# Optimization experiments

Measured on AMD Instinct MI355X. Metric: run time of the kernel, lower is better.

The kernel has to match this reference:

```python
import jax, jax.numpy as jnp
import numpy as np

V, H, B, T = 32000, 1024, 32, 256  # vocab, rnn_size, batch, seq_length


def setup_inputs() -> dict:
    key = jax.random.key(0)
    ks = jax.random.split(key, 6)
    s = 1.0 / np.sqrt(H)
    return {
        "input_data": jax.random.randint(ks[0], (B, T), 0, V, dtype=jnp.int32),
        "targets": jax.random.randint(ks[1], (B, T), 0, V, dtype=jnp.int32),
        "embedding": jax.random.uniform(ks[2], (V, H), minval=-1.0, maxval=1.0, dtype=jnp.float32),
        "softmax_b": jnp.zeros((V,), jnp.float32),
        "W0": (jax.random.normal(ks[3], (2 * H, 4 * H)) * s).astype(jnp.float32),
        "b0": jnp.zeros((4 * H,), jnp.float32),
        "W1": (jax.random.normal(ks[4], (2 * H, 4 * H)) * s).astype(jnp.float32),
        "b1": jnp.zeros((4 * H,), jnp.float32),
    }


def _lstm_step(x, c, h, W, b):
    # TF LSTMCell: gates i, j, f, o; forget_bias = 1.0
    z = jnp.concatenate([x, h], axis=-1) @ W + b  # [B, 4H]
    i, j, f, o = jnp.split(z, 4, axis=-1)
    c2 = c * jax.nn.sigmoid(f + 1.0) + jax.nn.sigmoid(i) * jnp.tanh(j)
    h2 = jax.nn.sigmoid(o) * jnp.tanh(c2)
    return c2, h2


def reference(input_data, targets, embedding, softmax_b, W0, b0, W1, b1):
    x = embedding[input_data]  # [B, T, H]
    Bb, Hh = x.shape[0], embedding.shape[1]
    zeros = jnp.zeros((Bb, Hh), x.dtype)
    init = ((zeros, zeros), (zeros, zeros))  # ((c0,h0),(c1,h1))

    def step(carry, xt):
        (c0, h0), (c1, h1) = carry
        c0, h0 = _lstm_step(xt, c0, h0, W0, b0)
        c1, h1 = _lstm_step(h0, c1, h1, W1, b1)
        return ((c0, h0), (c1, h1)), h1

    _, outs = jax.lax.scan(step, init, jnp.swapaxes(x, 0, 1))  # [T, B, H]
    output = jnp.swapaxes(outs, 0, 1).reshape(-1, Hh)  # [B*T, H]
    logits = output @ embedding.T + softmax_b  # tied softmax weights, [B*T, V]
    labels = targets.reshape(-1)
    logp = jax.nn.log_softmax(logits)
    loss = -jnp.take_along_axis(logp, labels[:, None], axis=1)[:, 0]
    cost = jnp.sum(loss) / Bb
    return logits, cost
```

## Files before the change

kernel.cpp:

```cpp
#include <hip/hip_runtime.h>
#include <hip/hip_bf16.h>

#define DEV static __device__ __forceinline__

typedef unsigned short u16;
typedef unsigned long long u64;
typedef __attribute__((ext_vector_type(8))) short short8;
typedef __attribute__((ext_vector_type(4))) float f32x4;

constexpr int V = 32000, H = 1024, B = 32, T = 256;
constexpr int BT = B * T;
constexpr int G  = 4 * H;
constexpr int NCH = V / 256;
constexpr int NWG2 = 256;
constexpr int RSTRIDE = 32 * 2048 + 2048;

constexpr size_t SZ_WT    = (size_t)G * 2048 * 2;
constexpr size_t OFF_W0T  = 0;
constexpr size_t OFF_W1T  = OFF_W0T + SZ_WT;
constexpr size_t OFF_EBF  = OFF_W1T + SZ_WT;
constexpr size_t OFF_XBF  = OFF_EBF + (size_t)V * H * 2;
constexpr size_t OFF_XP0  = OFF_XBF + (size_t)BT * H * 2;
constexpr size_t OFF_H1   = OFF_XP0 + (size_t)BT * G * 2;
constexpr size_t OFF_HSEQ = OFF_H1 + (size_t)BT * H * 2;
constexpr size_t SZ_HSEQ  = (size_t)(T + 2) * RSTRIDE * 2;
constexpr size_t OFF_SYNC = OFF_HSEQ + SZ_HSEQ;
constexpr size_t SZ_SYNC  = (size_t)2 * 256 * 128 * 4;
constexpr size_t OFF_PMAX = OFF_SYNC + SZ_SYNC;
constexpr size_t OFF_PSUM = OFF_PMAX + (size_t)BT * NCH * 4;
constexpr size_t OFF_LOSS = OFF_PSUM + (size_t)BT * NCH * 4;

DEV u16 f2bf(float x) {
  union { float f; unsigned int u; } v; v.f = x;
  unsigned int r = v.u + 0x7fffu + ((v.u >> 16) & 1u);
  return (u16)(r >> 16);
}
DEV float bf2f(u16 b) {
  union { unsigned int u; float f; } v; v.u = ((unsigned int)b) << 16;
  return v.f;
}
DEV float sigm(float x) { return 1.f / (1.f + expf(-x)); }

DEV void gload_lds16(const u16* g, u16* l) {
  __builtin_amdgcn_global_load_lds(
      (__attribute__((address_space(1))) void*)g,
      (__attribute__((address_space(3))) void*)l, 16, 0, 0);
}


__global__ void k_transpose_cvt(const float* __restrict__ in, u16* __restrict__ out,
                                int R, int C) {
  __shared__ float tile[32][33];
  int bc = blockIdx.x * 32, br = blockIdx.y * 32;
  int tx = threadIdx.x & 31, ty0 = threadIdx.x >> 5;
#pragma unroll
  for (int i = 0; i < 4; ++i) {
    int ty = ty0 + i * 8;
    tile[ty][tx] = in[(size_t)(br + ty) * C + bc + tx];
  }
  __syncthreads();
#pragma unroll
  for (int i = 0; i < 4; ++i) {
    int ty = ty0 + i * 8;
    out[(size_t)(bc + ty) * R + br + tx] = f2bf(tile[tx][ty]);
  }
}

__global__ void k_cvt_bf16(const float* __restrict__ in, u16* __restrict__ out, int n4) {
  int i = blockIdx.x * blockDim.x + threadIdx.x;
  int stride = gridDim.x * blockDim.x;
  for (; i < n4; i += stride) {
    float4 v = ((const float4*)in)[i];
    ushort4 o;
    o.x = f2bf(v.x); o.y = f2bf(v.y); o.z = f2bf(v.z); o.w = f2bf(v.w);
    ((ushort4*)out)[i] = o;
  }
}

__global__ void k_gather_x(const float* __restrict__ emb, const int* __restrict__ inp,
                           u16* __restrict__ Xbf) {
  int row = blockIdx.x;
  int t = row >> 5, b = row & 31;
  int tok = inp[b * T + t];
  const float4* src = (const float4*)(emb + (size_t)tok * H);
  ushort4* dst = (ushort4*)(Xbf + (size_t)row * H);
  float4 v = src[threadIdx.x];
  ushort4 o;
  o.x = f2bf(v.x); o.y = f2bf(v.y); o.z = f2bf(v.z); o.w = f2bf(v.w);
  dst[threadIdx.x] = o;
}

__global__ void k_zero(unsigned int* __restrict__ p, int nwords) {
  int i = blockIdx.x * blockDim.x + threadIdx.x;
  int stride = gridDim.x * blockDim.x;
  for (; i < nwords; i += stride) p[i] = 0u;
}

template <int CMODE>
__global__ __launch_bounds__(256)
void k_gemm(const u16* __restrict__ A, int lda,
            const u16* __restrict__ Bt, int ldb,
            float* __restrict__ C, int ldc,
            const float* __restrict__ bias, int K) {
  __shared__ alignas(16) u16 ldsA[128 * 32];
  __shared__ alignas(16) u16 ldsB[128 * 32];

  unsigned nwg = gridDim.x * gridDim.y;
  unsigned flat = blockIdx.y * gridDim.x + blockIdx.x;
  unsigned nf = (flat & 7) * (nwg >> 3) + (flat >> 3);
  unsigned bx = nf % gridDim.x, by = nf / gridDim.x;

  int tid = threadIdx.x, lane = tid & 63, w = tid >> 6;
  int row0 = by * 128, col0 = bx * 128;
  int wr = w >> 1, wc = w & 1;
  int c15 = lane & 15, q4 = lane >> 4;

  const u16* ag[2]; const u16* bg[2];
#pragma unroll
  for (int j = 0; j < 2; ++j) {
    int r = (j * 4 + w) * 16 + (lane >> 2);
    int k = (lane & 3) * 8;
    ag[j] = A + (size_t)(row0 + r) * lda + k;
    bg[j] = Bt + (size_t)(col0 + r) * ldb + k;
  }
  u16* lA0 = ldsA + (size_t)(0 + w) * 512;
  u16* lA1 = ldsA + (size_t)(4 + w) * 512;
  u16* lB0 = ldsB + (size_t)(0 + w) * 512;
  u16* lB1 = ldsB + (size_t)(4 + w) * 512;

  f32x4 acc[4][4];
#pragma unroll
  for (int m = 0; m < 4; ++m)
#pragma unroll
    for (int n = 0; n < 4; ++n) acc[m][n] = (f32x4){0.f, 0.f, 0.f, 0.f};

  int nk = K >> 5;
  for (int kk = 0; kk < nk; ++kk) {
    int kb = kk * 32;
    gload_lds16(ag[0] + kb, lA0);
    gload_lds16(ag[1] + kb, lA1);
    gload_lds16(bg[0] + kb, lB0);
    gload_lds16(bg[1] + kb, lB1);
    __syncthreads();

    short8 af[4], bfr[4];
#pragma unroll
    for (int m = 0; m < 4; ++m)
      af[m] = *(const short8*)(ldsA + (wr * 64 + m * 16 + c15) * 32 + q4 * 8);
#pragma unroll
    for (int n = 0; n < 4; ++n)
      bfr[n] = *(const short8*)(ldsB + (wc * 64 + n * 16 + c15) * 32 + q4 * 8);
#pragma unroll
    for (int m = 0; m < 4; ++m)
#pragma unroll
      for (int n = 0; n < 4; ++n)
        acc[m][n] = __builtin_amdgcn_mfma_f32_16x16x32_bf16(af[m], bfr[n], acc[m][n], 0, 0, 0);
    __syncthreads();
  }

  float bias_n[4];
#pragma unroll
  for (int n = 0; n < 4; ++n) bias_n[n] = bias[col0 + wc * 64 + n * 16 + c15];

#pragma unroll
  for (int m = 0; m < 4; ++m) {
#pragma unroll
    for (int jr = 0; jr < 4; ++jr) {
      int r_g = row0 + wr * 64 + m * 16 + q4 * 4 + jr;
#pragma unroll
      for (int n = 0; n < 4; ++n) {
        int c_g = col0 + wc * 64 + n * 16 + c15;
        float val = acc[m][n][jr] + bias_n[n];
        if (CMODE == 0) {
          C[(size_t)r_g * ldc + c_g] = val;
        } else {
          int tt = r_g >> 5, bb = r_g & 31;
          int q = c_g >> 10, wgup = (c_g & 1023) >> 3, uu = c_g & 7;
          ((u16*)C)[((((size_t)tt * 128 + wgup) * 32 + bb) * 32) + q * 8 + uu] = f2bf(val);
        }
      }
    }
  }
}

constexpr int GNT = 32;

DEV void stage_half256(const u16* __restrict__ A, int lda,
                       const u16* __restrict__ Bt, int ldb,
                       int row0, int col0, u16* lds, int Hh, int tid) {
  int t = Hh >> 2, j = Hh & 3, op = j >> 1, hh = j & 1;
  int wid = tid >> 6, lane = tid & 63;
  int r = hh * 128 + wid * 16 + (lane >> 2);
  int k = t * 32 + (((lane & 3) ^ ((lane >> 2) & 3)) << 3);
  const u16* g = (op == 0) ? (A + (size_t)(row0 + r) * lda + k)
                           : (Bt + (size_t)(col0 + r) * ldb + k);
  u16* l = lds + (size_t)((op * 2 + (t & 1)) * 8192 + (hh * 128 + wid * 16) * 32);
  gload_lds16(g, l);
}

template <bool SM_EPI>
__global__ __launch_bounds__(512)
void k_gemm256(const u16* __restrict__ A, int lda,
               const u16* __restrict__ Bt, int ldb,
               float* __restrict__ C, int ldc,
               const float* __restrict__ bias,
               float* __restrict__ pmax, float* __restrict__ psum, int nch) {
  __shared__ alignas(16) u16 lds[4 * 8192];

  unsigned nwg = gridDim.x * gridDim.y;
  unsigned flat = blockIdx.y * gridDim.x + blockIdx.x;
  unsigned nf = (flat & 7) * (nwg >> 3) + (flat >> 3);
  int bx = nf % gridDim.x, by = nf / gridDim.x;
  int row0 = by * 256, col0 = bx * 256;

  int tid = threadIdx.x, lane = tid & 63, wid = tid >> 6;
  int wr = wid >> 2, wc = wid & 3;
  int c15 = lane & 15, q4 = lane >> 4;
  int usw = (q4 ^ (c15 & 3)) << 3;

  f32x4 acc[8][4];
#pragma unroll
  for (int m = 0; m < 8; ++m)
#pragma unroll
    for (int n = 0; n < 4; ++n) acc[m][n] = (f32x4){0.f, 0.f, 0.f, 0.f};

#pragma unroll
  for (int h = 0; h < 7; ++h)
    stage_half256(A, lda, Bt, ldb, row0, col0, lds, h, tid);
  asm volatile("s_waitcnt vmcnt(3)" ::: "memory");
  __builtin_amdgcn_sched_barrier(0);
  __builtin_amdgcn_s_barrier();

  int Hh = 7;
  short8 af[4], bfr[4];

  for (int t = 0; t < GNT; ++t) {
    int pt = t & 1;
    const u16* la = lds + pt * 8192;
    const u16* lb = lds + (2 + pt) * 8192;

#pragma unroll
    for (int m = 0; m < 4; ++m)
      af[m] = *(const short8*)(la + (wr * 128 + m * 16 + c15) * 32 + usw);
#pragma unroll
    for (int n = 0; n < 4; ++n)
      bfr[n] = *(const short8*)(lb + (wc * 64 + n * 16 + c15) * 32 + usw);
    if (Hh < 4 * GNT) { stage_half256(A, lda, Bt, ldb, row0, col0, lds, Hh, tid); ++Hh; }
    if (Hh < 4 * GNT) { stage_half256(A, lda, Bt, ldb, row0, col0, lds, Hh, tid); ++Hh; }
    __builtin_amdgcn_s_barrier();
    asm volatile("s_waitcnt lgkmcnt(0)" ::: "memory");
    __builtin_amdgcn_sched_barrier(0);
    __builtin_amdgcn_s_setprio(1);
#pragma unroll
    for (int m = 0; m < 4; ++m)
#pragma unroll
      for (int n = 0; n < 4; ++n)
        acc[m][n] = __builtin_amdgcn_mfma_f32_16x16x32_bf16(af[m], bfr[n], acc[m][n], 0, 0, 0);
    __builtin_amdgcn_s_setprio(0);
    __builtin_amdgcn_s_barrier();

#pragma unroll
    for (int m = 0; m < 4; ++m)
      af[m] = *(const short8*)(la + (wr * 128 + (m + 4) * 16 + c15) * 32 + usw);
    if (Hh < 4 * GNT) { stage_half256(A, lda, Bt, ldb, row0, col0, lds, Hh, tid); ++Hh; }
    if (Hh < 4 * GNT) { stage_half256(A, lda, Bt, ldb, row0, col0, lds, Hh, tid); ++Hh; }
    __builtin_amdgcn_s_barrier();
    asm volatile("s_waitcnt lgkmcnt(0)" ::: "memory");
    __builtin_amdgcn_sched_barrier(0);
    __builtin_amdgcn_s_setprio(1);
#pragma unroll
    for (int m = 0; m < 4; ++m)
#pragma unroll
      for (int n = 0; n < 4; ++n)
        acc[m + 4][n] = __builtin_amdgcn_mfma_f32_16x16x32_bf16(af[m], bfr[n], acc[m + 4][n], 0, 0, 0);
    __builtin_amdgcn_s_setprio(0);
    if (t < GNT - 2) {
      asm volatile("s_waitcnt vmcnt(3)" ::: "memory");
      __builtin_amdgcn_sched_barrier(0);
    } else if (t == GNT - 2) {
      asm volatile("s_waitcnt vmcnt(0)" ::: "memory");
      __builtin_amdgcn_sched_barrier(0);
    }
    __builtin_amdgcn_s_barrier();
  }

  float bias_n[4];
#pragma unroll
  for (int n = 0; n < 4; ++n) bias_n[n] = bias[col0 + wc * 64 + n * 16 + c15];

  float2* red = (float2*)lds;
  __syncthreads();

#pragma unroll
  for (int m = 0; m < 8; ++m) {
#pragma unroll
    for (int jr = 0; jr < 4; ++jr) {
      int rloc = wr * 128 + m * 16 + q4 * 4 + jr;
      int r_g = row0 + rloc;
      float v[4];
#pragma unroll
      for (int n = 0; n < 4; ++n) {
        int c_g = col0 + wc * 64 + n * 16 + c15;
        float val = acc[m][n][jr] + bias_n[n];
        C[(size_t)r_g * ldc + c_g] = val;
        v[n] = val;
      }
      if (SM_EPI) {
        float mx = fmaxf(fmaxf(v[0], v[1]), fmaxf(v[2], v[3]));
        float s = __expf(v[0] - mx) + __expf(v[1] - mx) + __expf(v[2] - mx) + __expf(v[3] - mx);
#pragma unroll
        for (int d = 1; d < 16; d <<= 1) {
          float mo = __shfl_xor(mx, d, 64);
          float so = __shfl_xor(s, d, 64);
          float M2 = fmaxf(mx, mo);
          s = s * __expf(mx - M2) + so * __expf(mo - M2);
          mx = M2;
        }
        if (c15 == 0) red[rloc * 4 + wc] = make_float2(mx, s);
      }
    }
  }
  if (SM_EPI) {
    __syncthreads();
    if (tid < 256) {
      float M = -1e30f, S = 0.f;
#pragma unroll
      for (int i = 0; i < 4; ++i) {
        float2 a = red[tid * 4 + i];
        float M2 = fmaxf(M, a.x);
        S = S * __expf(M - M2) + a.y * __expf(a.x - M2);
        M = M2;
      }
      pmax[(size_t)(row0 + tid) * nch + bx] = M;
      psum[(size_t)(row0 + tid) * nch + bx] = S;
    }
  }
}


#define RED(w_, bt_, nt_, r_, c_) red[((((w_)*2 + (bt_)) * 2 + (nt_)) * 16 + (r_)) * 16 + (c_)]

DEV void wait_flags(const int* __restrict__ fa, const int* __restrict__ fb) {
  if (threadIdx.x < 64) {
    int lane = threadIdx.x;
    while (true) {
      int ok = 1;
      if (fa) {
        int a0 = __hip_atomic_load(fa + lane,      __ATOMIC_RELAXED, __HIP_MEMORY_SCOPE_AGENT);
        int a1 = __hip_atomic_load(fa + 64 + lane, __ATOMIC_RELAXED, __HIP_MEMORY_SCOPE_AGENT);
        ok &= (a0 != 0) & (a1 != 0);
      }
      if (fb) {
        int b0 = __hip_atomic_load(fb + lane,      __ATOMIC_RELAXED, __HIP_MEMORY_SCOPE_AGENT);
        int b1 = __hip_atomic_load(fb + 64 + lane, __ATOMIC_RELAXED, __HIP_MEMORY_SCOPE_AGENT);
        ok &= (b0 != 0) & (b1 != 0);
      }
      if (__all(ok)) break;
      __builtin_amdgcn_s_sleep(1);
    }
  }
  __builtin_amdgcn_sched_barrier(0);
  __syncthreads();
}

DEV void publish_flag(int* __restrict__ word) {
  __syncthreads();
  if (threadIdx.x == 0)
    __hip_atomic_store(word, 1, __ATOMIC_RELAXED, __HIP_MEMORY_SCOPE_AGENT);
}

template <int KH, bool IS_L0>
DEV void lstm_role(const u16* __restrict__ WT,
                   const u16* __restrict__ xp0p,
                   const float* __restrict__ zb1,
                   u16* __restrict__ hseq, u16* __restrict__ H1bf,
                   int* __restrict__ f0, int* __restrict__ f1,
                   float* __restrict__ red, int wgu) {
  constexpr int KOFF = IS_L0 ? 1024 : 0;
  constexpr int KS = KH / 4;
  constexpr int NKC = KS / 32;
  int tid = threadIdx.x, lane = tid & 63, w = tid >> 6;
  int c15 = lane & 15, q4 = lane >> 4;
  int eb = tid >> 3, eu = tid & 7;

  short8 wfr[2][NKC];
#pragma unroll
  for (int nt = 0; nt < 2; ++nt) {
    int lr = nt * 16 + c15;
    const u16* rp = WT + (size_t)((lr >> 3) * 1024 + wgu * 8 + (lr & 7)) * 2048
                    + KOFF + w * KS + q4 * 8;
#pragma unroll
    for (int kc = 0; kc < NKC; ++kc)
      wfr[nt][kc] = *(const short8*)(rp + kc * 32);
  }

  float zpc[4];
  if (!IS_L0) {
#pragma unroll
    for (int q = 0; q < 4; ++q) zpc[q] = zb1[q * 1024 + wgu * 8 + eu];
  }
  float creg = 0.f;

  for (int it_t = 0; it_t < T; ++it_t) {
    int t = IS_L0 ? it_t : it_t + 1;

    float zp[4];
    if (IS_L0) {
#pragma unroll
      for (int q = 0; q < 4; ++q)
        zp[q] = bf2f(xp0p[((((size_t)t * 128 + wgu) * 32 + eb) * 32) + q * 8 + eu]);
    } else {
#pragma unroll
      for (int q = 0; q < 4; ++q) zp[q] = zpc[q];
    }

    if (IS_L0) {
      if (t >= 1) wait_flags(f0 + (size_t)(t - 1) * 128, nullptr);
    } else {
      wait_flags(f0 + (size_t)(t - 1) * 128,
                 t >= 2 ? f1 + (size_t)(t - 2) * 128 : nullptr);
    }

    const u16* hread = hseq + (size_t)t * RSTRIDE;
    f32x4 acc[2][2];
#pragma unroll
    for (int bt = 0; bt < 2; ++bt)
#pragma unroll
      for (int nt = 0; nt < 2; ++nt) acc[bt][nt] = (f32x4){0.f, 0.f, 0.f, 0.f};

#pragma unroll
    for (int kc = 0; kc < NKC; ++kc) {
      int kh = w * KS + kc * 32 + q4 * 8;
      short8 a0 = *(const short8*)(hread + (size_t)c15 * 2048 + kh);
      short8 a1 = *(const short8*)(hread + (size_t)(16 + c15) * 2048 + kh);
      acc[0][0] = __builtin_amdgcn_mfma_f32_16x16x32_bf16(a0, wfr[0][kc], acc[0][0], 0, 0, 0);
      acc[0][1] = __builtin_amdgcn_mfma_f32_16x16x32_bf16(a0, wfr[1][kc], acc[0][1], 0, 0, 0);
      acc[1][0] = __builtin_amdgcn_mfma_f32_16x16x32_bf16(a1, wfr[0][kc], acc[1][0], 0, 0, 0);
      acc[1][1] = __builtin_amdgcn_mfma_f32_16x16x32_bf16(a1, wfr[1][kc], acc[1][1], 0, 0, 0);
    }

#pragma unroll
    for (int bt = 0; bt < 2; ++bt)
#pragma unroll
      for (int nt = 0; nt < 2; ++nt)
#pragma unroll
        for (int jr = 0; jr < 4; ++jr)
          RED(w, bt, nt, q4 * 4 + jr, c15) = acc[bt][nt][jr];
    __syncthreads();

    int bt = eb >> 4, rr = eb & 15;
    float z[4];
#pragma unroll
    for (int q = 0; q < 4; ++q) {
      int lr = q * 8 + eu, nt = lr >> 4, cc = lr & 15;
      z[q] = RED(0, bt, nt, rr, cc) + RED(1, bt, nt, rr, cc) +
             RED(2, bt, nt, rr, cc) + RED(3, bt, nt, rr, cc) + zp[q];
    }
    float gi = sigm(z[0]);
    float gj = tanhf(z[1]);
    float gf = sigm(z[2] + 1.f);
    float go = sigm(z[3]);
    creg = creg * gf + gi * gj;
    float hv = go * tanhf(creg);

    int hb = (int)f2bf(hv);
    int hp = __shfl_xor(hb, 1, 64);
    if (!(tid & 1)) {
      unsigned int pack = (unsigned int)(u16)hb | ((unsigned int)(u16)hp << 16);
      u16* hwr = hseq + (size_t)(t + 1) * RSTRIDE + (IS_L0 ? 0 : 1024);
      __hip_atomic_store((unsigned int*)(hwr + (size_t)eb * 2048 + wgu * 8 + eu), pack,
                         __ATOMIC_RELAXED, __HIP_MEMORY_SCOPE_AGENT);
      if (!IS_L0)
        __builtin_nontemporal_store(pack,
            (unsigned int*)(H1bf + ((size_t)eb * T + (t - 1)) * H + wgu * 8 + eu));
    }

    publish_flag(IS_L0 ? (f0 + (size_t)t * 128 + wgu)
                       : (f1 + (size_t)(t - 1) * 128 + wgu));
  }
}

__global__ __launch_bounds__(256, 1)
void k_lstm_persistent(const u16* __restrict__ W0T, const u16* __restrict__ W1T,
                       const u16* __restrict__ xp0p, const float* __restrict__ b1,
                       u16* __restrict__ hseq, u16* __restrict__ H1bf,
                       int* __restrict__ sync) {
  __shared__ float red[4 * 2 * 2 * 16 * 16];
  int* f0 = sync;
  int* f1 = sync + 256 * 128;
  int wg = blockIdx.x;
  if (wg < 128)
    lstm_role<1024, true>(W0T, xp0p, nullptr, hseq, H1bf, f0, f1, red, wg);
  else
    lstm_role<2048, false>(W1T, nullptr, b1, hseq, H1bf, f0, f1, red, wg - 128);
}

__global__ void k_rowfin(const float* __restrict__ pmax, const float* __restrict__ psum,
                         const float* __restrict__ Cl, const int* __restrict__ targets,
                         float* __restrict__ loss) {
  int row = blockIdx.x;
  int tid = threadIdx.x, lane = tid & 63, w = tid >> 6;
  float mx = -1e30f, s = 0.f;
  if (tid < NCH) { mx = pmax[(size_t)row * NCH + tid]; s = psum[(size_t)row * NCH + tid]; }
#pragma unroll
  for (int d = 1; d < 64; d <<= 1) {
    float mo = __shfl_xor(mx, d, 64);
    float so = __shfl_xor(s, d, 64);
    float M2 = fmaxf(mx, mo);
    s = s * __expf(mx - M2) + so * __expf(mo - M2);
    mx = M2;
  }
  __shared__ float2 wred[4];
  if (lane == 0) wred[w] = make_float2(mx, s);
  __syncthreads();
  if (tid == 0) {
    float M = wred[0].x, S = wred[0].y;
#pragma unroll
    for (int i = 1; i < 4; ++i) {
      float M2 = fmaxf(M, wred[i].x);
      S = S * __expf(M - M2) + wred[i].y * __expf(wred[i].x - M2);
      M = M2;
    }
    float logZ = M + logf(S);
    int tgt = targets[row];
    float xt = Cl[(size_t)row * V + tgt];
    loss[row] = logZ - xt;
  }
}

__global__ void k_cost(const float* __restrict__ loss, float* __restrict__ out) {
  int tid = threadIdx.x, lane = tid & 63, w = tid >> 6;
  float s = 0.f;
  for (int i = tid; i < BT; i += 256) s += loss[i];
#pragma unroll
  for (int d = 1; d < 64; d <<= 1) s += __shfl_xor(s, d, 64);
  __shared__ float ws4[4];
  if (lane == 0) ws4[w] = s;
  __syncthreads();
  if (tid == 0) out[0] = (ws4[0] + ws4[1] + ws4[2] + ws4[3]) * (1.0f / B);
}

extern "C" void kernel_launch(void* const* d_in, const int* in_sizes, int n_in,
                              void* d_out, int out_size, void* d_ws, size_t ws_size,
                              hipStream_t stream) {
  const int*   input_data = (const int*)d_in[0];
  const int*   targets    = (const int*)d_in[1];
  const float* emb        = (const float*)d_in[2];
  const float* softmax_b  = (const float*)d_in[3];
  const float* W0         = (const float*)d_in[4];
  const float* b0         = (const float*)d_in[5];
  const float* W1         = (const float*)d_in[6];
  const float* b1         = (const float*)d_in[7];
  float* out = (float*)d_out;
  char*  ws  = (char*)d_ws;

  u16*   W0T  = (u16*)(ws + OFF_W0T);
  u16*   W1T  = (u16*)(ws + OFF_W1T);
  u16*   Ebf  = (u16*)(ws + OFF_EBF);
  u16*   Xbf  = (u16*)(ws + OFF_XBF);
  u16*   xp0p = (u16*)(ws + OFF_XP0);
  u16*   H1bf = (u16*)(ws + OFF_H1);
  u16*   hseq = (u16*)(ws + OFF_HSEQ);
  int*   sync = (int*)(ws + OFF_SYNC);
  float* pmax = (float*)(ws + OFF_PMAX);
  float* psum = (float*)(ws + OFF_PSUM);
  float* lossb= (float*)(ws + OFF_LOSS);

  k_transpose_cvt<<<dim3(G / 32, 2048 / 32), 256, 0, stream>>>(W0, W0T, 2048, G);
  k_transpose_cvt<<<dim3(G / 32, 2048 / 32), 256, 0, stream>>>(W1, W1T, 2048, G);
  k_cvt_bf16<<<2048, 256, 0, stream>>>(emb, Ebf, V * H / 4);
  k_gather_x<<<BT, 256, 0, stream>>>(emb, input_data, Xbf);
  k_zero<<<64, 256, 0, stream>>>((unsigned int*)(ws + OFF_HSEQ), RSTRIDE);
  k_zero<<<64, 256, 0, stream>>>((unsigned int*)(ws + OFF_SYNC), (int)(SZ_SYNC / 4));

  k_gemm<1><<<dim3(G / 128, BT / 128), 256, 0, stream>>>(
      Xbf, H, W0T, 2048, (float*)xp0p, G, b0, H);

  k_lstm_persistent<<<dim3(NWG2), dim3(256), 0, stream>>>(
      W0T, W1T, xp0p, b1, hseq, H1bf, sync);

  k_gemm256<true><<<dim3(V / 256, BT / 256), 512, 0, stream>>>(
      H1bf, H, Ebf, H, out, V, softmax_b, pmax, psum, NCH);

  k_rowfin<<<BT, 256, 0, stream>>>(pmax, psum, out, targets, lossb);
  k_cost<<<1, 256, 0, stream>>>(lossb, out + (size_t)BT * V);
}
```

Measured before the change: 2.991 ms.

## Split LSTM batch into two independent chains and triple-buffer logits GEMM LDS

The persistent LSTM kernel now processes the batch as two independent 16-row halves, each with its own hidden-state buffer and flag arrays. One half's matmul and gate work can proceed while the other half waits on its inter-workgroup flags, hiding part of the per-step synchronization latency. The cost is twice as many flag waits and barriers per timestep, with the gate epilogue running on only half the threads. Separately, the vocab-projection GEMM moves from double to triple LDS buffering with a two-tile prefetch distance, at the cost of more shared memory per block.

```diff
diff --git a/kernel.cpp b/kernel.cpp
--- a/kernel.cpp
+++ b/kernel.cpp
@@ -13,7 +13,7 @@
 constexpr int G  = 4 * H;
 constexpr int NCH = V / 256;
 constexpr int NWG2 = 256;
-constexpr int RSTRIDE = 32 * 2048 + 2048;
+constexpr int RST2 = 16 * 2048 + 1024;
 
 constexpr size_t SZ_WT    = (size_t)G * 2048 * 2;
 constexpr size_t OFF_W0T  = 0;
@@ -23,9 +23,9 @@
 constexpr size_t OFF_XP0  = OFF_XBF + (size_t)BT * H * 2;
 constexpr size_t OFF_H1   = OFF_XP0 + (size_t)BT * G * 2;
 constexpr size_t OFF_HSEQ = OFF_H1 + (size_t)BT * H * 2;
-constexpr size_t SZ_HSEQ  = (size_t)(T + 2) * RSTRIDE * 2;
+constexpr size_t SZ_HSEQ  = (size_t)2 * (T + 2) * RST2 * 2;
 constexpr size_t OFF_SYNC = OFF_HSEQ + SZ_HSEQ;
-constexpr size_t SZ_SYNC  = (size_t)2 * 256 * 128 * 4;
+constexpr size_t SZ_SYNC  = (size_t)2 * 2 * 256 * 128 * 4;
 constexpr size_t OFF_PMAX = OFF_SYNC + SZ_SYNC;
 constexpr size_t OFF_PSUM = OFF_PMAX + (size_t)BT * NCH * 4;
 constexpr size_t OFF_LOSS = OFF_PSUM + (size_t)BT * NCH * 4;
@@ -185,16 +185,16 @@
 
 constexpr int GNT = 32;
 
-DEV void stage_half256(const u16* __restrict__ A, int lda,
-                       const u16* __restrict__ Bt, int ldb,
-                       int row0, int col0, u16* lds, int Hh, int tid) {
-  int t = Hh >> 2, j = Hh & 3, op = j >> 1, hh = j & 1;
+DEV void stage256(const u16* __restrict__ A, int lda,
+                  const u16* __restrict__ Bt, int ldb,
+                  int row0, int col0, u16* lds, int t, int h, int tid) {
+  int op = h >> 1, hh = h & 1;
   int wid = tid >> 6, lane = tid & 63;
   int r = hh * 128 + wid * 16 + (lane >> 2);
   int k = t * 32 + (((lane & 3) ^ ((lane >> 2) & 3)) << 3);
   const u16* g = (op == 0) ? (A + (size_t)(row0 + r) * lda + k)
                            : (Bt + (size_t)(col0 + r) * ldb + k);
-  u16* l = lds + (size_t)((op * 2 + (t & 1)) * 8192 + (hh * 128 + wid * 16) * 32);
+  u16* l = lds + (size_t)((op * 3 + (t % 3)) * 8192 + (hh * 128 + wid * 16) * 32);
   gload_lds16(g, l);
 }
 
@@ -205,7 +205,7 @@
                float* __restrict__ C, int ldc,
                const float* __restrict__ bias,
                float* __restrict__ pmax, float* __restrict__ psum, int nch) {
-  __shared__ alignas(16) u16 lds[4 * 8192];
+  __shared__ alignas(16) u16 lds[6 * 8192];
 
   unsigned nwg = gridDim.x * gridDim.y;
   unsigned flat = blockIdx.y * gridDim.x + blockIdx.x;
@@ -225,19 +225,18 @@
     for (int n = 0; n < 4; ++n) acc[m][n] = (f32x4){0.f, 0.f, 0.f, 0.f};
 
 #pragma unroll
-  for (int h = 0; h < 7; ++h)
-    stage_half256(A, lda, Bt, ldb, row0, col0, lds, h, tid);
-  asm volatile("s_waitcnt vmcnt(3)" ::: "memory");
+  for (int h = 0; h < 4; ++h) stage256(A, lda, Bt, ldb, row0, col0, lds, 0, h, tid);
+#pragma unroll
+  for (int h = 0; h < 4; ++h) stage256(A, lda, Bt, ldb, row0, col0, lds, 1, h, tid);
+  asm volatile("s_waitcnt vmcnt(4)" ::: "memory");
   __builtin_amdgcn_sched_barrier(0);
   __builtin_amdgcn_s_barrier();
 
-  int Hh = 7;
   short8 af[4], bfr[4];
 
   for (int t = 0; t < GNT; ++t) {
-    int pt = t & 1;
-    const u16* la = lds + pt * 8192;
-    const u16* lb = lds + (2 + pt) * 8192;
+    const u16* la = lds + (size_t)(t % 3) * 8192;
+    const u16* lb = lds + (size_t)(3 + t % 3) * 8192;
 
 #pragma unroll
     for (int m = 0; m < 4; ++m)
@@ -245,8 +244,10 @@
 #pragma unroll
     for (int n = 0; n < 4; ++n)
       bfr[n] = *(const short8*)(lb + (wc * 64 + n * 16 + c15) * 32 + usw);
-    if (Hh < 4 * GNT) { stage_half256(A, lda, Bt, ldb, row0, col0, lds, Hh, tid); ++Hh; }
-    if (Hh < 4 * GNT) { stage_half256(A, lda, Bt, ldb, row0, col0, lds, Hh, tid); ++Hh; }
+    if (t + 2 < GNT) {
+      stage256(A, lda, Bt, ldb, row0, col0, lds, t + 2, 0, tid);
+      stage256(A, lda, Bt, ldb, row0, col0, lds, t + 2, 1, tid);
+    }
     __builtin_amdgcn_s_barrier();
     asm volatile("s_waitcnt lgkmcnt(0)" ::: "memory");
     __builtin_amdgcn_sched_barrier(0);
@@ -262,8 +263,10 @@
 #pragma unroll
     for (int m = 0; m < 4; ++m)
       af[m] = *(const short8*)(la + (wr * 128 + (m + 4) * 16 + c15) * 32 + usw);
-    if (Hh < 4 * GNT) { stage_half256(A, lda, Bt, ldb, row0, col0, lds, Hh, tid); ++Hh; }
-    if (Hh < 4 * GNT) { stage_half256(A, lda, Bt, ldb, row0, col0, lds, Hh, tid); ++Hh; }
+    if (t + 2 < GNT) {
+      stage256(A, lda, Bt, ldb, row0, col0, lds, t + 2, 2, tid);
+      stage256(A, lda, Bt, ldb, row0, col0, lds, t + 2, 3, tid);
+    }
     __builtin_amdgcn_s_barrier();
     asm volatile("s_waitcnt lgkmcnt(0)" ::: "memory");
     __builtin_amdgcn_sched_barrier(0);
@@ -275,7 +278,7 @@
         acc[m + 4][n] = __builtin_amdgcn_mfma_f32_16x16x32_bf16(af[m], bfr[n], acc[m + 4][n], 0, 0, 0);
     __builtin_amdgcn_s_setprio(0);
     if (t < GNT - 2) {
-      asm volatile("s_waitcnt vmcnt(3)" ::: "memory");
+      asm volatile("s_waitcnt vmcnt(4)" ::: "memory");
       __builtin_amdgcn_sched_barrier(0);
     } else if (t == GNT - 2) {
       asm volatile("s_waitcnt vmcnt(0)" ::: "memory");
@@ -338,7 +341,7 @@
 }
 
 
-#define RED(w_, bt_, nt_, r_, c_) red[((((w_)*2 + (bt_)) * 2 + (nt_)) * 16 + (r_)) * 16 + (c_)]
+#define RED3(w_, nt_, r_, c_) red[(((w_)*2 + (nt_)) * 16 + (r_)) * 16 + (c_)]
 
 DEV void wait_flags(const int* __restrict__ fa, const int* __restrict__ fb) {
   if (threadIdx.x < 64) {
@@ -361,12 +364,6 @@
   }
   __builtin_amdgcn_sched_barrier(0);
   __syncthreads();
-}
-
-DEV void publish_flag(int* __restrict__ word) {
-  __syncthreads();
-  if (threadIdx.x == 0)
-    __hip_atomic_store(word, 1, __ATOMIC_RELAXED, __HIP_MEMORY_SCOPE_AGENT);
 }
 
 template <int KH, bool IS_L0>
@@ -381,7 +378,8 @@
   constexpr int NKC = KS / 32;
   int tid = threadIdx.x, lane = tid & 63, w = tid >> 6;
   int c15 = lane & 15, q4 = lane >> 4;
-  int eb = tid >> 3, eu = tid & 7;
+  int eb = (tid >> 3) & 15, eu = tid & 7;
+  bool epi = tid < 128;
 
   short8 wfr[2][NKC];
 #pragma unroll
@@ -399,95 +397,99 @@
 #pragma unroll
     for (int q = 0; q < 4; ++q) zpc[q] = zb1[q * 1024 + wgu * 8 + eu];
   }
-  float creg = 0.f;
+  float cregs[2] = {0.f, 0.f};
 
   for (int it_t = 0; it_t < T; ++it_t) {
     int t = IS_L0 ? it_t : it_t + 1;
-
-    float zp[4];
-    if (IS_L0) {
-#pragma unroll
-      for (int q = 0; q < 4; ++q)
-        zp[q] = bf2f(xp0p[((((size_t)t * 128 + wgu) * 32 + eb) * 32) + q * 8 + eu]);
-    } else {
-#pragma unroll
-      for (int q = 0; q < 4; ++q) zp[q] = zpc[q];
-    }
-
-    if (IS_L0) {
-      if (t >= 1) wait_flags(f0 + (size_t)(t - 1) * 128, nullptr);
-    } else {
-      wait_flags(f0 + (size_t)(t - 1) * 128,
-                 t >= 2 ? f1 + (size_t)(t - 2) * 128 : nullptr);
-    }
-
-    const u16* hread = hseq + (size_t)t * RSTRIDE;
-    f32x4 acc[2][2];
-#pragma unroll
-    for (int bt = 0; bt < 2; ++bt)
-#pragma unroll
-      for (int nt = 0; nt < 2; ++nt) acc[bt][nt] = (f32x4){0.f, 0.f, 0.f, 0.f};
-
-#pragma unroll
-    for (int kc = 0; kc < NKC; ++kc) {
-      int kh = w * KS + kc * 32 + q4 * 8;
-      short8 a0 = *(const short8*)(hread + (size_t)c15 * 2048 + kh);
-      short8 a1 = *(const short8*)(hread + (size_t)(16 + c15) * 2048 + kh);
-      acc[0][0] = __builtin_amdgcn_mfma_f32_16x16x32_bf16(a0, wfr[0][kc], acc[0][0], 0, 0, 0);
-      acc[0][1] = __builtin_amdgcn_mfma_f32_16x16x32_bf16(a0, wfr[1][kc], acc[0][1], 0, 0, 0);
-      acc[1][0] = __builtin_amdgcn_mfma_f32_16x16x32_bf16(a1, wfr[0][kc], acc[1][0], 0, 0, 0);
-      acc[1][1] = __builtin_amdgcn_mfma_f32_16x16x32_bf16(a1, wfr[1][kc], acc[1][1], 0, 0, 0);
-    }
-
-#pragma unroll
-    for (int bt = 0; bt < 2; ++bt)
-#pragma unroll
-      for (int nt = 0; nt < 2; ++nt)
-#pragma unroll
-        for (int jr = 0; jr < 4; ++jr)
-          RED(w, bt, nt, q4 * 4 + jr, c15) = acc[bt][nt][jr];
-    __syncthreads();
-
-    int bt = eb >> 4, rr = eb & 15;
-    float z[4];
-#pragma unroll
-    for (int q = 0; q < 4; ++q) {
-      int lr = q * 8 + eu, nt = lr >> 4, cc = lr & 15;
-      z[q] = RED(0, bt, nt, rr, cc) + RED(1, bt, nt, rr, cc) +
-             RED(2, bt, nt, rr, cc) + RED(3, bt, nt, rr, cc) + zp[q];
-    }
-    float gi = sigm(z[0]);
-    float gj = tanhf(z[1]);
-    float gf = sigm(z[2] + 1.f);
-    float go = sigm(z[3]);
-    creg = creg * gf + gi * gj;
-    float hv = go * tanhf(creg);
-
-    int hb = (int)f2bf(hv);
-    int hp = __shfl_xor(hb, 1, 64);
-    if (!(tid & 1)) {
-      unsigned int pack = (unsigned int)(u16)hb | ((unsigned int)(u16)hp << 16);
-      u16* hwr = hseq + (size_t)(t + 1) * RSTRIDE + (IS_L0 ? 0 : 1024);
-      __hip_atomic_store((unsigned int*)(hwr + (size_t)eb * 2048 + wgu * 8 + eu), pack,
-                         __ATOMIC_RELAXED, __HIP_MEMORY_SCOPE_AGENT);
-      if (!IS_L0)
-        __builtin_nontemporal_store(pack,
-            (unsigned int*)(H1bf + ((size_t)eb * T + (t - 1)) * H + wgu * 8 + eu));
-    }
-
-    publish_flag(IS_L0 ? (f0 + (size_t)t * 128 + wgu)
-                       : (f1 + (size_t)(t - 1) * 128 + wgu));
+#pragma unroll
+    for (int c = 0; c < 2; ++c) {
+      float zp[4];
+      if (IS_L0) {
+        int b = c * 16 + eb;
+#pragma unroll
+        for (int q = 0; q < 4; ++q)
+          zp[q] = bf2f(xp0p[((((size_t)t * 128 + wgu) * 32 + b) * 32) + q * 8 + eu]);
+      } else {
+#pragma unroll
+        for (int q = 0; q < 4; ++q) zp[q] = zpc[q];
+      }
+
+      if (IS_L0) {
+        if (t >= 1) wait_flags(f0 + ((size_t)c * 256 + (t - 1)) * 128, nullptr);
+      } else {
+        wait_flags(f0 + ((size_t)c * 256 + (t - 1)) * 128,
+                   t >= 2 ? f1 + ((size_t)c * 256 + (t - 2)) * 128 : nullptr);
+      }
+
+      const u16* hread = hseq + ((size_t)c * (T + 2) + t) * RST2;
+      short8 afr[NKC];
+#pragma unroll
+      for (int kc = 0; kc < NKC; ++kc)
+        afr[kc] = *(const short8*)(hread + (size_t)c15 * 2048 + w * KS + kc * 32 + q4 * 8);
+
+      f32x4 acc0 = (f32x4){0.f, 0.f, 0.f, 0.f};
+      f32x4 acc1 = (f32x4){0.f, 0.f, 0.f, 0.f};
+#pragma unroll
+      for (int kc = 0; kc < NKC; ++kc) {
+        acc0 = __builtin_amdgcn_mfma_f32_16x16x32_bf16(afr[kc], wfr[0][kc], acc0, 0, 0, 0);
+        acc1 = __builtin_amdgcn_mfma_f32_16x16x32_bf16(afr[kc], wfr[1][kc], acc1, 0, 0, 0);
+      }
+
+#pragma unroll
+      for (int jr = 0; jr < 4; ++jr) {
+        RED3(w, 0, q4 * 4 + jr, c15) = acc0[jr];
+        RED3(w, 1, q4 * 4 + jr, c15) = acc1[jr];
+      }
+      __syncthreads();
+
+      if (epi) {
+        float z[4];
+#pragma unroll
+        for (int q = 0; q < 4; ++q) {
+          int lr = q * 8 + eu, nt = lr >> 4, cc = lr & 15;
+          z[q] = RED3(0, nt, eb, cc) + RED3(1, nt, eb, cc) +
+                 RED3(2, nt, eb, cc) + RED3(3, nt, eb, cc) + zp[q];
+        }
+        float gi = sigm(z[0]);
+        float gj = tanhf(z[1]);
+        float gf = sigm(z[2] + 1.f);
+        float go = sigm(z[3]);
+        cregs[c] = cregs[c] * gf + gi * gj;
+        float hv = go * tanhf(cregs[c]);
+
+        int hb = (int)f2bf(hv);
+        int hp = __shfl_xor(hb, 1, 64);
+        if (!(tid & 1)) {
+          unsigned int pack = (unsigned int)(u16)hb | ((unsigned int)(u16)hp << 16);
+          u16* hwr = hseq + ((size_t)c * (T + 2) + t + 1) * RST2 + (IS_L0 ? 0 : 1024);
+          __hip_atomic_store((unsigned int*)(hwr + (size_t)eb * 2048 + wgu * 8 + eu), pack,
+                             __ATOMIC_RELAXED, __HIP_MEMORY_SCOPE_AGENT);
+          if (!IS_L0) {
+            int b = c * 16 + eb;
+            __builtin_nontemporal_store(pack,
+                (unsigned int*)(H1bf + ((size_t)b * T + (t - 1)) * H + wgu * 8 + eu));
+          }
+        }
+      }
+
+      __syncthreads();
+      if (tid == 0) {
+        int* word = IS_L0 ? (f0 + ((size_t)c * 256 + t) * 128 + wgu)
+                          : (f1 + ((size_t)c * 256 + (t - 1)) * 128 + wgu);
+        __hip_atomic_store(word, 1, __ATOMIC_RELAXED, __HIP_MEMORY_SCOPE_AGENT);
+      }
+    }
   }
 }
 
 __global__ __launch_bounds__(256, 1)
-void k_lstm_persistent(const u16* __restrict__ W0T, const u16* __restrict__ W1T,
-                       const u16* __restrict__ xp0p, const float* __restrict__ b1,
-                       u16* __restrict__ hseq, u16* __restrict__ H1bf,
-                       int* __restrict__ sync) {
-  __shared__ float red[4 * 2 * 2 * 16 * 16];
+void k_lstm3(const u16* __restrict__ W0T, const u16* __restrict__ W1T,
+             const u16* __restrict__ xp0p, const float* __restrict__ b1,
+             u16* __restrict__ hseq, u16* __restrict__ H1bf,
+             int* __restrict__ sync) {
+  __shared__ float red[4 * 2 * 16 * 16];
   int* f0 = sync;
-  int* f1 = sync + 256 * 128;
+  int* f1 = sync + 2 * 256 * 128;
   int wg = blockIdx.x;
   if (wg < 128)
     lstm_role<1024, true>(W0T, xp0p, nullptr, hseq, H1bf, f0, f1, red, wg);
@@ -570,13 +572,15 @@
   k_transpose_cvt<<<dim3(G / 32, 2048 / 32), 256, 0, stream>>>(W1, W1T, 2048, G);
   k_cvt_bf16<<<2048, 256, 0, stream>>>(emb, Ebf, V * H / 4);
   k_gather_x<<<BT, 256, 0, stream>>>(emb, input_data, Xbf);
-  k_zero<<<64, 256, 0, stream>>>((unsigned int*)(ws + OFF_HSEQ), RSTRIDE);
+  k_zero<<<32, 256, 0, stream>>>((unsigned int*)(ws + OFF_HSEQ), RST2);
+  k_zero<<<32, 256, 0, stream>>>(
+      (unsigned int*)(ws + OFF_HSEQ + (size_t)(T + 2) * RST2 * 2), RST2);
   k_zero<<<64, 256, 0, stream>>>((unsigned int*)(ws + OFF_SYNC), (int)(SZ_SYNC / 4));
 
   k_gemm<1><<<dim3(G / 128, BT / 128), 256, 0, stream>>>(
       Xbf, H, W0T, 2048, (float*)xp0p, G, b0, H);
 
-  k_lstm_persistent<<<dim3(NWG2), dim3(256), 0, stream>>>(
+  k_lstm3<<<dim3(NWG2), dim3(256), 0, stream>>>(
       W0T, W1T, xp0p, b1, hseq, H1bf, sync);
 
   k_gemm256<true><<<dim3(V / 256, BT / 256), 512, 0, stream>>>(
```

Result: no change. 2.993 ms (+0.1%).

## Triple-buffer GEMM pipeline, reuse it for input projection, merge and slim small kernels

Applied to the files above, without the earlier changes.

The 256-tile GEMM moves from a double-buffered LDS ring with a half-tile stage counter to a triple-buffered ring that prefetches two K-steps ahead. The same kernel now also handles the layer-0 input projection, replacing the smaller 128-tile GEMM. The two weight-transpose launches become one launch using blockIdx.z. The LSTM spin-wait drops its s_sleep, and k_rowfin now gives each row one wavefront with no LDS reduction. Together these aim to cut pipeline stalls, launch count and idle polling, at the cost of more LDS per block (which may lower occupancy) and busier spinning.

```diff
diff --git a/kernel.cpp b/kernel.cpp
--- a/kernel.cpp
+++ b/kernel.cpp
@@ -48,21 +48,23 @@
 }
 
 
-__global__ void k_transpose_cvt(const float* __restrict__ in, u16* __restrict__ out,
-                                int R, int C) {
+__global__ void k_transpose_cvt2(const float* __restrict__ in0, u16* __restrict__ out0,
+                                 const float* __restrict__ in1, u16* __restrict__ out1) {
+  const float* in = blockIdx.z ? in1 : in0;
+  u16* out = blockIdx.z ? out1 : out0;
   __shared__ float tile[32][33];
   int bc = blockIdx.x * 32, br = blockIdx.y * 32;
   int tx = threadIdx.x & 31, ty0 = threadIdx.x >> 5;
 #pragma unroll
   for (int i = 0; i < 4; ++i) {
     int ty = ty0 + i * 8;
-    tile[ty][tx] = in[(size_t)(br + ty) * C + bc + tx];
+    tile[ty][tx] = in[(size_t)(br + ty) * G + bc + tx];
   }
   __syncthreads();
 #pragma unroll
   for (int i = 0; i < 4; ++i) {
     int ty = ty0 + i * 8;
-    out[(size_t)(bc + ty) * R + br + tx] = f2bf(tile[tx][ty]);
+    out[(size_t)(bc + ty) * 2048 + br + tx] = f2bf(tile[tx][ty]);
   }
 }
 
@@ -96,216 +98,138 @@
   for (; i < nwords; i += stride) p[i] = 0u;
 }
 
-template <int CMODE>
-__global__ __launch_bounds__(256)
-void k_gemm(const u16* __restrict__ A, int lda,
-            const u16* __restrict__ Bt, int ldb,
-            float* __restrict__ C, int ldc,
-            const float* __restrict__ bias, int K) {
-  __shared__ alignas(16) u16 ldsA[128 * 32];
-  __shared__ alignas(16) u16 ldsB[128 * 32];
+constexpr int GNT = 32;
+
+DEV void stage256(const u16* __restrict__ A, int lda,
+                  const u16* __restrict__ Bt, int ldb,
+                  int row0, int col0, u16* lds, int t, int h, int tid) {
+  int op = h >> 1, hh = h & 1;
+  int wid = tid >> 6, lane = tid & 63;
+  int r = hh * 128 + wid * 16 + (lane >> 2);
+  int k = t * 32 + (((lane & 3) ^ ((lane >> 2) & 3)) << 3);
+  const u16* g = (op == 0) ? (A + (size_t)(row0 + r) * lda + k)
+                           : (Bt + (size_t)(col0 + r) * ldb + k);
+  u16* l = lds + (size_t)((op * 3 + (t % 3)) * 8192 + (hh * 128 + wid * 16) * 32);
+  gload_lds16(g, l);
+}
+
+template <int MODE>
+__global__ __launch_bounds__(512)
+void k_gemm256(const u16* __restrict__ A, int lda,
+               const u16* __restrict__ Bt, int ldb,
+               float* __restrict__ C, int ldc,
+               const float* __restrict__ bias,
+               float* __restrict__ pmax, float* __restrict__ psum, int nch) {
+  __shared__ alignas(16) u16 lds[6 * 8192];
 
   unsigned nwg = gridDim.x * gridDim.y;
   unsigned flat = blockIdx.y * gridDim.x + blockIdx.x;
   unsigned nf = (flat & 7) * (nwg >> 3) + (flat >> 3);
-  unsigned bx = nf % gridDim.x, by = nf / gridDim.x;
-
-  int tid = threadIdx.x, lane = tid & 63, w = tid >> 6;
-  int row0 = by * 128, col0 = bx * 128;
-  int wr = w >> 1, wc = w & 1;
+  int bx = nf % gridDim.x, by = nf / gridDim.x;
+  int row0 = by * 256, col0 = bx * 256;
+
+  int tid = threadIdx.x, lane = tid & 63, wid = tid >> 6;
+  int wr = wid >> 2, wc = wid & 3;
   int c15 = lane & 15, q4 = lane >> 4;
-
-  const u16* ag[2]; const u16* bg[2];
-#pragma unroll
-  for (int j = 0; j < 2; ++j) {
-    int r = (j * 4 + w) * 16 + (lane >> 2);
-    int k = (lane & 3) * 8;
-    ag[j] = A + (size_t)(row0 + r) * lda + k;
-    bg[j] = Bt + (size_t)(col0 + r) * ldb + k;
-  }
-  u16* lA0 = ldsA + (size_t)(0 + w) * 512;
-  u16* lA1 = ldsA + (size_t)(4 + w) * 512;
-  u16* lB0 = ldsB + (size_t)(0 + w) * 512;
-  u16* lB1 = ldsB + (size_t)(4 + w) * 512;
-
-  f32x4 acc[4][4];
-#pragma unroll
-  for (int m = 0; m < 4; ++m)
+  int usw = (q4 ^ (c15 & 3)) << 3;
+
+  f32x4 acc[8][4];
+#pragma unroll
+  for (int m = 0; m < 8; ++m)
 #pragma unroll
     for (int n = 0; n < 4; ++n) acc[m][n] = (f32x4){0.f, 0.f, 0.f, 0.f};
 
-  int nk = K >> 5;
-  for (int kk = 0; kk < nk; ++kk) {
-    int kb = kk * 32;
-    gload_lds16(ag[0] + kb, lA0);
-    gload_lds16(ag[1] + kb, lA1);
-    gload_lds16(bg[0] + kb, lB0);
-    gload_lds16(bg[1] + kb, lB1);
-    __syncthreads();
-
-    short8 af[4], bfr[4];
+#pragma unroll
+  for (int h = 0; h < 4; ++h) stage256(A, lda, Bt, ldb, row0, col0, lds, 0, h, tid);
+#pragma unroll
+  for (int h = 0; h < 4; ++h) stage256(A, lda, Bt, ldb, row0, col0, lds, 1, h, tid);
+  asm volatile("s_waitcnt vmcnt(4)" ::: "memory");
+  __builtin_amdgcn_sched_barrier(0);
+  __builtin_amdgcn_s_barrier();
+
+  short8 af[4], bfr[4];
+
+  for (int t = 0; t < GNT; ++t) {
+    const u16* la = lds + (size_t)(t % 3) * 8192;
+    const u16* lb = lds + (size_t)(3 + t % 3) * 8192;
+
 #pragma unroll
     for (int m = 0; m < 4; ++m)
-      af[m] = *(const short8*)(ldsA + (wr * 64 + m * 16 + c15) * 32 + q4 * 8);
+      af[m] = *(const short8*)(la + (wr * 128 + m * 16 + c15) * 32 + usw);
 #pragma unroll
     for (int n = 0; n < 4; ++n)
-      bfr[n] = *(const short8*)(ldsB + (wc * 64 + n * 16 + c15) * 32 + q4 * 8);
+      bfr[n] = *(const short8*)(lb + (wc * 64 + n * 16 + c15) * 32 + usw);
+    if (t + 2 < GNT) {
+      stage256(A, lda, Bt, ldb, row0, col0, lds, t + 2, 0, tid);
+      stage256(A, lda, Bt, ldb, row0, col0, lds, t + 2, 1, tid);
+    }
+    __builtin_amdgcn_s_barrier();
+    asm volatile("s_waitcnt lgkmcnt(0)" ::: "memory");
+    __builtin_amdgcn_sched_barrier(0);
+    __builtin_amdgcn_s_setprio(1);
 #pragma unroll
     for (int m = 0; m < 4; ++m)
 #pragma unroll
       for (int n = 0; n < 4; ++n)
         acc[m][n] = __builtin_amdgcn_mfma_f32_16x16x32_bf16(af[m], bfr[n], acc[m][n], 0, 0, 0);
-    __syncthreads();
+    __builtin_amdgcn_s_setprio(0);
+    __builtin_amdgcn_s_barrier();
+
+#pragma unroll
+    for (int m = 0; m < 4; ++m)
+      af[m] = *(const short8*)(la + (wr * 128 + (m + 4) * 16 + c15) * 32 + usw);
+    if (t + 2 < GNT) {
+      stage256(A, lda, Bt, ldb, row0, col0, lds, t + 2, 2, tid);
+      stage256(A, lda, Bt, ldb, row0, col0, lds, t + 2, 3, tid);
+    }
+    __builtin_amdgcn_s_barrier();
+    asm volatile("s_waitcnt lgkmcnt(0)" ::: "memory");
+    __builtin_amdgcn_sched_barrier(0);
+    __builtin_amdgcn_s_setprio(1);
+#pragma unroll
+    for (int m = 0; m < 4; ++m)
+#pragma unroll
+      for (int n = 0; n < 4; ++n)
+        acc[m + 4][n] = __builtin_amdgcn_mfma_f32_16x16x32_bf16(af[m], bfr[n], acc[m + 4][n], 0, 0, 0);
+    __builtin_amdgcn_s_setprio(0);
+    if (t < GNT - 2) {
+      asm volatile("s_waitcnt vmcnt(4)" ::: "memory");
+      __builtin_amdgcn_sched_barrier(0);
+    } else if (t == GNT - 2) {
+      asm volatile("s_waitcnt vmcnt(0)" ::: "memory");
+      __builtin_amdgcn_sched_barrier(0);
+    }
+    __builtin_amdgcn_s_barrier();
   }
 
   float bias_n[4];
 #pragma unroll
   for (int n = 0; n < 4; ++n) bias_n[n] = bias[col0 + wc * 64 + n * 16 + c15];
 
-#pragma unroll
-  for (int m = 0; m < 4; ++m) {
+  float2* red = (float2*)lds;
+  __syncthreads();
+
+#pragma unroll
+  for (int m = 0; m < 8; ++m) {
 #pragma unroll
     for (int jr = 0; jr < 4; ++jr) {
-      int r_g = row0 + wr * 64 + m * 16 + q4 * 4 + jr;
+      int rloc = wr * 128 + m * 16 + q4 * 4 + jr;
+      int r_g = row0 + rloc;
+      float v[4];
 #pragma unroll
       for (int n = 0; n < 4; ++n) {
         int c_g = col0 + wc * 64 + n * 16 + c15;
         float val = acc[m][n][jr] + bias_n[n];
-        if (CMODE == 0) {
+        if (MODE == 1) {
           C[(size_t)r_g * ldc + c_g] = val;
         } else {
           int tt = r_g >> 5, bb = r_g & 31;
           int q = c_g >> 10, wgup = (c_g & 1023) >> 3, uu = c_g & 7;
           ((u16*)C)[((((size_t)tt * 128 + wgup) * 32 + bb) * 32) + q * 8 + uu] = f2bf(val);
         }
-      }
-    }
-  }
-}
-
-constexpr int GNT = 32;
-
-DEV void stage_half256(const u16* __restrict__ A, int lda,
-                       const u16* __restrict__ Bt, int ldb,
-                       int row0, int col0, u16* lds, int Hh, int tid) {
-  int t = Hh >> 2, j = Hh & 3, op = j >> 1, hh = j & 1;
-  int wid = tid >> 6, lane = tid & 63;
-  int r = hh * 128 + wid * 16 + (lane >> 2);
-  int k = t * 32 + (((lane & 3) ^ ((lane >> 2) & 3)) << 3);
-  const u16* g = (op == 0) ? (A + (size_t)(row0 + r) * lda + k)
-                           : (Bt + (size_t)(col0 + r) * ldb + k);
-  u16* l = lds + (size_t)((op * 2 + (t & 1)) * 8192 + (hh * 128 + wid * 16) * 32);
-  gload_lds16(g, l);
-}
-
-template <bool SM_EPI>
-__global__ __launch_bounds__(512)
-void k_gemm256(const u16* __restrict__ A, int lda,
-               const u16* __restrict__ Bt, int ldb,
-               float* __restrict__ C, int ldc,
-               const float* __restrict__ bias,
-               float* __restrict__ pmax, float* __restrict__ psum, int nch) {
-  __shared__ alignas(16) u16 lds[4 * 8192];
-
-  unsigned nwg = gridDim.x * gridDim.y;
-  unsigned flat = blockIdx.y * gridDim.x + blockIdx.x;
-  unsigned nf = (flat & 7) * (nwg >> 3) + (flat >> 3);
-  int bx = nf % gridDim.x, by = nf / gridDim.x;
-  int row0 = by * 256, col0 = bx * 256;
-
-  int tid = threadIdx.x, lane = tid & 63, wid = tid >> 6;
-  int wr = wid >> 2, wc = wid & 3;
-  int c15 = lane & 15, q4 = lane >> 4;
-  int usw = (q4 ^ (c15 & 3)) << 3;
-
-  f32x4 acc[8][4];
-#pragma unroll
-  for (int m = 0; m < 8; ++m)
-#pragma unroll
-    for (int n = 0; n < 4; ++n) acc[m][n] = (f32x4){0.f, 0.f, 0.f, 0.f};
-
-#pragma unroll
-  for (int h = 0; h < 7; ++h)
-    stage_half256(A, lda, Bt, ldb, row0, col0, lds, h, tid);
-  asm volatile("s_waitcnt vmcnt(3)" ::: "memory");
-  __builtin_amdgcn_sched_barrier(0);
-  __builtin_amdgcn_s_barrier();
-
-  int Hh = 7;
-  short8 af[4], bfr[4];
-
-  for (int t = 0; t < GNT; ++t) {
-    int pt = t & 1;
-    const u16* la = lds + pt * 8192;
-    const u16* lb = lds + (2 + pt) * 8192;
-
-#pragma unroll
-    for (int m = 0; m < 4; ++m)
-      af[m] = *(const short8*)(la + (wr * 128 + m * 16 + c15) * 32 + usw);
-#pragma unroll
-    for (int n = 0; n < 4; ++n)
-      bfr[n] = *(const short8*)(lb + (wc * 64 + n * 16 + c15) * 32 + usw);
-    if (Hh < 4 * GNT) { stage_half256(A, lda, Bt, ldb, row0, col0, lds, Hh, tid); ++Hh; }
-    if (Hh < 4 * GNT) { stage_half256(A, lda, Bt, ldb, row0, col0, lds, Hh, tid); ++Hh; }
-    __builtin_amdgcn_s_barrier();
-    asm volatile("s_waitcnt lgkmcnt(0)" ::: "memory");
-    __builtin_amdgcn_sched_barrier(0);
-    __builtin_amdgcn_s_setprio(1);
-#pragma unroll
-    for (int m = 0; m < 4; ++m)
-#pragma unroll
-      for (int n = 0; n < 4; ++n)
-        acc[m][n] = __builtin_amdgcn_mfma_f32_16x16x32_bf16(af[m], bfr[n], acc[m][n], 0, 0, 0);
-    __builtin_amdgcn_s_setprio(0);
-    __builtin_amdgcn_s_barrier();
-
-#pragma unroll
-    for (int m = 0; m < 4; ++m)
-      af[m] = *(const short8*)(la + (wr * 128 + (m + 4) * 16 + c15) * 32 + usw);
-    if (Hh < 4 * GNT) { stage_half256(A, lda, Bt, ldb, row0, col0, lds, Hh, tid); ++Hh; }
-    if (Hh < 4 * GNT) { stage_half256(A, lda, Bt, ldb, row0, col0, lds, Hh, tid); ++Hh; }
-    __builtin_amdgcn_s_barrier();
-    asm volatile("s_waitcnt lgkmcnt(0)" ::: "memory");
-    __builtin_amdgcn_sched_barrier(0);
-    __builtin_amdgcn_s_setprio(1);
-#pragma unroll
-    for (int m = 0; m < 4; ++m)
-#pragma unroll
-      for (int n = 0; n < 4; ++n)
-        acc[m + 4][n] = __builtin_amdgcn_mfma_f32_16x16x32_bf16(af[m], bfr[n], acc[m + 4][n], 0, 0, 0);
-    __builtin_amdgcn_s_setprio(0);
-    if (t < GNT - 2) {
-      asm volatile("s_waitcnt vmcnt(3)" ::: "memory");
-      __builtin_amdgcn_sched_barrier(0);
-    } else if (t == GNT - 2) {
-      asm volatile("s_waitcnt vmcnt(0)" ::: "memory");
-      __builtin_amdgcn_sched_barrier(0);
-    }
-    __builtin_amdgcn_s_barrier();
-  }
-
-  float bias_n[4];
-#pragma unroll
-  for (int n = 0; n < 4; ++n) bias_n[n] = bias[col0 + wc * 64 + n * 16 + c15];
-
-  float2* red = (float2*)lds;
-  __syncthreads();
-
-#pragma unroll
-  for (int m = 0; m < 8; ++m) {
-#pragma unroll
-    for (int jr = 0; jr < 4; ++jr) {
-      int rloc = wr * 128 + m * 16 + q4 * 4 + jr;
-      int r_g = row0 + rloc;
-      float v[4];
-#pragma unroll
-      for (int n = 0; n < 4; ++n) {
-        int c_g = col0 + wc * 64 + n * 16 + c15;
-        float val = acc[m][n][jr] + bias_n[n];
-        C[(size_t)r_g * ldc + c_g] = val;
         v[n] = val;
       }
-      if (SM_EPI) {
+      if (MODE == 1) {
         float mx = fmaxf(fmaxf(v[0], v[1]), fmaxf(v[2], v[3]));
         float s = __expf(v[0] - mx) + __expf(v[1] - mx) + __expf(v[2] - mx) + __expf(v[3] - mx);
 #pragma unroll
@@ -320,7 +244,7 @@
       }
     }
   }
-  if (SM_EPI) {
+  if (MODE == 1) {
     __syncthreads();
     if (tid < 256) {
       float M = -1e30f, S = 0.f;
@@ -356,7 +280,6 @@
         ok &= (b0 != 0) & (b1 != 0);
       }
       if (__all(ok)) break;
-      __builtin_amdgcn_s_sleep(1);
     }
   }
   __builtin_amdgcn_sched_barrier(0);
@@ -498,10 +421,17 @@
 __global__ void k_rowfin(const float* __restrict__ pmax, const float* __restrict__ psum,
                          const float* __restrict__ Cl, const int* __restrict__ targets,
                          float* __restrict__ loss) {
-  int row = blockIdx.x;
-  int tid = threadIdx.x, lane = tid & 63, w = tid >> 6;
+  int lane = threadIdx.x & 63, wv = threadIdx.x >> 6;
+  int row = blockIdx.x * 4 + wv;
   float mx = -1e30f, s = 0.f;
-  if (tid < NCH) { mx = pmax[(size_t)row * NCH + tid]; s = psum[(size_t)row * NCH + tid]; }
+  if (lane < NCH) { mx = pmax[(size_t)row * NCH + lane]; s = psum[(size_t)row * NCH + lane]; }
+  if (lane + 64 < NCH) {
+    float m2 = pmax[(size_t)row * NCH + 64 + lane];
+    float s2 = psum[(size_t)row * NCH + 64 + lane];
+    float M2 = fmaxf(mx, m2);
+    s = s * __expf(mx - M2) + s2 * __expf(m2 - M2);
+    mx = M2;
+  }
 #pragma unroll
   for (int d = 1; d < 64; d <<= 1) {
     float mo = __shfl_xor(mx, d, 64);
@@ -510,18 +440,8 @@
     s = s * __expf(mx - M2) + so * __expf(mo - M2);
     mx = M2;
   }
-  __shared__ float2 wred[4];
-  if (lane == 0) wred[w] = make_float2(mx, s);
-  __syncthreads();
-  if (tid == 0) {
-    float M = wred[0].x, S = wred[0].y;
-#pragma unroll
-    for (int i = 1; i < 4; ++i) {
-      float M2 = fmaxf(M, wred[i].x);
-      S = S * __expf(M - M2) + wred[i].y * __expf(wred[i].x - M2);
-      M = M2;
-    }
-    float logZ = M + logf(S);
+  if (lane == 0) {
+    float logZ = mx + logf(s);
     int tgt = targets[row];
     float xt = Cl[(size_t)row * V + tgt];
     loss[row] = logZ - xt;
@@ -566,22 +486,21 @@
   float* psum = (float*)(ws + OFF_PSUM);
   float* lossb= (float*)(ws + OFF_LOSS);
 
-  k_transpose_cvt<<<dim3(G / 32, 2048 / 32), 256, 0, stream>>>(W0, W0T, 2048, G);
-  k_transpose_cvt<<<dim3(G / 32, 2048 / 32), 256, 0, stream>>>(W1, W1T, 2048, G);
+  k_transpose_cvt2<<<dim3(G / 32, 2048 / 32, 2), 256, 0, stream>>>(W0, W0T, W1, W1T);
   k_cvt_bf16<<<2048, 256, 0, stream>>>(emb, Ebf, V * H / 4);
   k_gather_x<<<BT, 256, 0, stream>>>(emb, input_data, Xbf);
   k_zero<<<64, 256, 0, stream>>>((unsigned int*)(ws + OFF_HSEQ), RSTRIDE);
   k_zero<<<64, 256, 0, stream>>>((unsigned int*)(ws + OFF_SYNC), (int)(SZ_SYNC / 4));
 
-  k_gemm<1><<<dim3(G / 128, BT / 128), 256, 0, stream>>>(
-      Xbf, H, W0T, 2048, (float*)xp0p, G, b0, H);
+  k_gemm256<0><<<dim3(G / 256, BT / 256), 512, 0, stream>>>(
+      Xbf, H, W0T, 2048, (float*)xp0p, 0, b0, nullptr, nullptr, 0);
 
   k_lstm_persistent<<<dim3(NWG2), dim3(256), 0, stream>>>(
       W0T, W1T, xp0p, b1, hseq, H1bf, sync);
 
-  k_gemm256<true><<<dim3(V / 256, BT / 256), 512, 0, stream>>>(
+  k_gemm256<1><<<dim3(V / 256, BT / 256), 512, 0, stream>>>(
       H1bf, H, Ebf, H, out, V, softmax_b, pmax, psum, NCH);
 
-  k_rowfin<<<BT, 256, 0, stream>>>(pmax, psum, out, targets, lossb);
+  k_rowfin<<<BT / 4, 256, 0, stream>>>(pmax, psum, out, targets, lossb);
   k_cost<<<1, 256, 0, stream>>>(lossb, out + (size_t)BT * V);
 }
```

Result: faster. 2.852 ms (-4.6%).
